# Kernel optimization log

Hardware: AMD Instinct MI355X
Metric: run time of the kernel (lower is better)

## Reference

```python
import jax, jax.numpy as jnp
import numpy as np

N = 100000      # nodes
E_RAND = 1500000
IN_DIM = 128
OUT_DIM = 128
H = 8
D = OUT_DIM // H  # 16 per-head dim
EPS = 1e-5


def _bn(x, gamma, beta):
    # BatchNorm1d, training mode: biased batch statistics over the node dim
    mu = jnp.mean(x, axis=0)
    var = jnp.mean((x - mu) ** 2, axis=0)
    return (x - mu) * jax.lax.rsqrt(var + EPS) * gamma + beta


def setup_inputs() -> dict:
    key = jax.random.key(0)
    ks = jax.random.split(key, 12)
    h = jax.random.normal(ks[0], (N, IN_DIM), dtype=jnp.float32)
    # edge list: random edges + self-loops so every dst has in-degree >= 1
    src_r = jax.random.randint(ks[1], (E_RAND,), 0, N, dtype=jnp.int32)
    dst_r = jax.random.randint(ks[2], (E_RAND,), 0, N, dtype=jnp.int32)
    loops = jnp.arange(N, dtype=jnp.int32)
    src = jnp.concatenate([loops, src_r])
    dst = jnp.concatenate([loops, dst_r])
    s = 1.0 / np.sqrt(IN_DIM)
    Wq = jax.random.normal(ks[3], (IN_DIM, OUT_DIM), dtype=jnp.float32) * s
    Wk = jax.random.normal(ks[4], (IN_DIM, OUT_DIM), dtype=jnp.float32) * s
    Wv = jax.random.normal(ks[5], (IN_DIM, OUT_DIM), dtype=jnp.float32) * s
    Wo = jax.random.normal(ks[6], (OUT_DIM, OUT_DIM), dtype=jnp.float32) * s
    bo = jnp.zeros((OUT_DIM,), dtype=jnp.float32)
    gamma1 = jnp.ones((OUT_DIM,), dtype=jnp.float32)
    beta1 = jnp.zeros((OUT_DIM,), dtype=jnp.float32)
    Wf1 = jax.random.normal(ks[7], (OUT_DIM, 2 * OUT_DIM), dtype=jnp.float32) * s
    bf1 = jnp.zeros((2 * OUT_DIM,), dtype=jnp.float32)
    Wf2 = jax.random.normal(ks[8], (2 * OUT_DIM, OUT_DIM), dtype=jnp.float32) * (1.0 / np.sqrt(2 * OUT_DIM))
    bf2 = jnp.zeros((OUT_DIM,), dtype=jnp.float32)
    gamma2 = jnp.ones((OUT_DIM,), dtype=jnp.float32)
    beta2 = jnp.zeros((OUT_DIM,), dtype=jnp.float32)
    return {"h": h, "Wq": Wq, "Wk": Wk, "Wv": Wv, "Wo": Wo, "bo": bo,
            "gamma1": gamma1, "beta1": beta1, "Wf1": Wf1, "bf1": bf1,
            "Wf2": Wf2, "bf2": bf2, "gamma2": gamma2, "beta2": beta2,
            "src": src, "dst": dst}


def reference(h, Wq, Wk, Wv, Wo, bo, gamma1, beta1, Wf1, bf1, Wf2, bf2,
              gamma2, beta2, src, dst):
    n = h.shape[0]
    Q = (h @ Wq).reshape(n, H, D)
    K = (h @ Wk).reshape(n, H, D)
    V = (h @ Wv).reshape(n, H, D)
    # per-edge score: (K[src] * Q[dst]).sum(-1), scaled exp with clamp
    score = jnp.sum(K[src] * Q[dst], axis=-1) / np.sqrt(D)   # [E, H]
    score = jnp.exp(jnp.clip(score, -5.0, 5.0))
    # weighted aggregation to dst nodes
    wV = jax.ops.segment_sum(V[src] * score[:, :, None], dst, num_segments=n)  # [N,H,D]
    z = jax.ops.segment_sum(score, dst, num_segments=n)                         # [N,H]
    attn = (wV / z[:, :, None]).reshape(n, OUT_DIM)
    # output projection + residual + batchnorm
    x = h + (attn @ Wo + bo)
    x = _bn(x, gamma1, beta1)
    # FFN + residual + batchnorm
    y = jax.nn.relu(x @ Wf1 + bf1) @ Wf2 + bf2
    x = _bn(x + y, gamma2, beta2)
    return x
```

## Files before the change

### kernel.cpp

```cpp
#include <hip/hip_runtime.h>

#define EPS 1e-5f
#define VSCALE 20.0f

typedef __attribute__((ext_vector_type(8))) short sh8;
typedef __attribute__((ext_vector_type(4))) float f4;
typedef __attribute__((ext_vector_type(2))) _Float16 h2f;

static __device__ __forceinline__ unsigned short f2b(float f) {
    union { float f; unsigned u; } v; v.f = f;
    unsigned r = v.u + 0x7FFF + ((v.u >> 16) & 1);
    return (unsigned short)(r >> 16);
}
static __device__ __forceinline__ float b2f(unsigned short b) {
    union { unsigned u; float f; } v; v.u = ((unsigned)b) << 16; return v.f;
}
static __device__ __forceinline__ unsigned pk2(float a, float b) {
    return (unsigned)f2b(a) | ((unsigned)f2b(b) << 16);
}
static __device__ __forceinline__ h2f u2h(unsigned u) {
    union { unsigned u; h2f h; } c; c.u = u; return c.h;
}
static __device__ __forceinline__ unsigned pkh2(float a, float b) {
    union { h2f h; unsigned u; } c;
    c.h.x = (_Float16)a; c.h.y = (_Float16)b;
    return c.u;
}
static __device__ __forceinline__ float dot2h(h2f a, h2f b, float c) {
#if __has_builtin(__builtin_amdgcn_fdot2)
    return __builtin_amdgcn_fdot2(a, b, c, false);
#else
    return (float)a.x * (float)b.x + (float)a.y * (float)b.y + c;
#endif
}
#if __has_builtin(__builtin_amdgcn_cvt_f32_ubyte0)
#define UB0(x) __builtin_amdgcn_cvt_f32_ubyte0(x)
#define UB1(x) __builtin_amdgcn_cvt_f32_ubyte1(x)
#define UB2(x) __builtin_amdgcn_cvt_f32_ubyte2(x)
#define UB3(x) __builtin_amdgcn_cvt_f32_ubyte3(x)
#else
#define UB0(x) ((float)((x) & 0xffu))
#define UB1(x) ((float)(((x) >> 8) & 0xffu))
#define UB2(x) ((float)(((x) >> 16) & 0xffu))
#define UB3(x) ((float)((x) >> 24))
#endif

static __device__ __forceinline__ void barrier_raw() {
    __builtin_amdgcn_sched_barrier(0);
    asm volatile("s_waitcnt lgkmcnt(0)" ::: "memory");
    __builtin_amdgcn_s_barrier();
    __builtin_amdgcn_sched_barrier(0);
}

__global__ __launch_bounds__(256) void prep_all_k(
    const float* __restrict__ Wq, const float* __restrict__ Wk,
    const float* __restrict__ Wv, const float* __restrict__ Wo,
    const float* __restrict__ Wf1, const float* __restrict__ Wf2,
    unsigned short* __restrict__ Wt)
{
    int i = blockIdx.x * 256 + threadIdx.x;
    if (i < 65536) {
        int s = i >> 14;
        const float* W = (s == 0) ? Wq : (s == 1) ? Wk : (s == 2) ? Wv : Wo;
        int l = i & 16383, k = l >> 7, n = l & 127;
        Wt[(i & ~16383) + n * 128 + k] = f2b(W[l]);
    } else if (i < 98304) {
        int l = i - 65536, k = l >> 8, n = l & 255;
        Wt[65536 + n * 128 + k] = f2b(Wf1[l]);
    } else {
        int l = i - 98304, k = l >> 7, n = l & 127;
        Wt[98304 + n * 256 + k] = f2b(Wf2[l]);
    }
}

__global__ __launch_bounds__(512, 4) void qkv3_k(
    const float* __restrict__ h, const unsigned short* __restrict__ Wt,
    _Float16* __restrict__ Qh, unsigned char* __restrict__ KV,
    int M, int tiles)
{
    constexpr int KD = 128, PER = 2;
    __shared__ __align__(16) unsigned short As[2][64 * KD];
    const int tid = threadIdx.x;
    const int wave = tid >> 6, lane = tid & 63;
    const int q = lane >> 4, lm = lane & 15;
    const int wr = wave >> 2, wc = wave & 3;
    const int wv = blockIdx.y;
    const unsigned short* Wblk = Wt + (size_t)wv * 16384;

    float4 rAf[PER][2];
    {
        const int rowT = blockIdx.x * 64;
#pragma unroll
        for (int i = 0; i < PER; ++i) {
            int g = tid + i * 512;
            int row = g >> 4, ch = g & 15;
            int grow = rowT + row; if (grow >= M) grow = M - 1;
            const float* p = &h[(size_t)grow * 128 + ch * 8];
            rAf[i][0] = *(const float4*)p;
            rAf[i][1] = *(const float4*)(p + 4);
        }
    }

    sh8 wfr[2][4];
#pragma unroll
    for (int ni = 0; ni < 2; ++ni)
#pragma unroll
        for (int kc = 0; kc < 4; ++kc)
            wfr[ni][kc] = *(const sh8*)&Wblk[(size_t)(wc * 32 + ni * 16 + lm) * KD
                                             + (kc * 4 + q) * 8];

    int cur = 0;
    for (int t = blockIdx.x; t < tiles; t += gridDim.x) {
        const int rowT = t * 64;
        barrier_raw();
        unsigned short* Asc = As[cur];
#pragma unroll
        for (int i = 0; i < PER; ++i) {
            int g = tid + i * 512;
            int row = g >> 4, ch = g & 15;
            uint4 v;
            v.x = pk2(rAf[i][0].x, rAf[i][0].y);
            v.y = pk2(rAf[i][0].z, rAf[i][0].w);
            v.z = pk2(rAf[i][1].x, rAf[i][1].y);
            v.w = pk2(rAf[i][1].z, rAf[i][1].w);
            *(uint4*)&Asc[row * KD + ((ch ^ (row & 7)) * 8)] = v;
        }
        const int tn = t + (int)gridDim.x;
        if (tn < tiles) {
            const int rowTn = tn * 64;
#pragma unroll
            for (int i = 0; i < PER; ++i) {
                int g = tid + i * 512;
                int row = g >> 4, ch = g & 15;
                int grow = rowTn + row; if (grow >= M) grow = M - 1;
                const float* p = &h[(size_t)grow * 128 + ch * 8];
                rAf[i][0] = *(const float4*)p;
                rAf[i][1] = *(const float4*)(p + 4);
            }
        }
        barrier_raw();

        f4 acc[2][2];
#pragma unroll
        for (int mi = 0; mi < 2; ++mi)
#pragma unroll
            for (int ni = 0; ni < 2; ++ni) {
                f4 z = {0.f, 0.f, 0.f, 0.f};
                acc[mi][ni] = z;
            }
#pragma unroll
        for (int kc = 0; kc < 4; ++kc) {
            sh8 af[2];
#pragma unroll
            for (int mi = 0; mi < 2; ++mi) {
                const int row = wr * 32 + mi * 16 + lm;
                af[mi] = *(const sh8*)&Asc[row * KD + (((kc * 4 + q) ^ (row & 7)) * 8)];
            }
#pragma unroll
            for (int mi = 0; mi < 2; ++mi)
#pragma unroll
                for (int ni = 0; ni < 2; ++ni)
                    acc[mi][ni] = __builtin_amdgcn_mfma_f32_16x16x32_bf16(
                        wfr[ni][kc], af[mi], acc[mi][ni], 0, 0, 0);
        }

#pragma unroll
        for (int mi = 0; mi < 2; ++mi) {
            const int row = rowT + wr * 32 + mi * 16 + lm;
            if (row >= M) continue;
#pragma unroll
            for (int ni = 0; ni < 2; ++ni) {
                const int col0 = wc * 32 + ni * 16 + q * 4;
                const f4 a = acc[mi][ni];
                if (wv == 0) {
                    uint2 o;
                    o.x = pkh2(a[0], a[1]);
                    o.y = pkh2(a[2], a[3]);
                    *(uint2*)&Qh[(size_t)row * 128 + col0] = o;
                } else if (wv == 1) {
                    uint2 o;
                    o.x = pkh2(a[0], a[1]);
                    o.y = pkh2(a[2], a[3]);
                    *(uint2*)(KV + (size_t)row * 384 + col0 * 2) = o;
                } else {
                    unsigned ob = 0;
#pragma unroll
                    for (int r = 0; r < 4; ++r) {
                        float tt = rintf(a[r] * VSCALE);
                        tt = fminf(fmaxf(tt, -127.f), 127.f);
                        ob |= ((unsigned)(unsigned char)(int)(tt + 128.f)) << (r * 8);
                    }
                    *(unsigned*)(KV + (size_t)row * 384 + 256 + col0) = ob;
                }
            }
        }
        cur ^= 1;
    }
}

template<int KD, int RES, int STATS, int RELU>
__global__ __launch_bounds__(512, 4) void gemm3_k(
    const unsigned short* __restrict__ A, const unsigned short* __restrict__ Wt,
    const float* __restrict__ bias, const void* __restrict__ resid,
    unsigned short* __restrict__ C, int M, int ldc, int tiles,
    const float* __restrict__ aff1, float* __restrict__ ostats)
{
    constexpr int CPR = KD / 8;
    constexpr int NWC = (KD == 128) ? 4 : 8;
    constexpr int NI  = (KD == 128) ? 2 : 1;
    constexpr int TM  = (KD == 128) ? 64 : 32;
    constexpr int PER = TM * CPR / 512;
    constexpr int KC  = KD / 32;
    __shared__ __align__(16) unsigned short As[2][TM * KD];
    __shared__ float sacc[256];
    const int tid = threadIdx.x;
    const int wave = tid >> 6, lane = tid & 63;
    const int q = lane >> 4, lm = lane & 15;
    const int wr = wave / NWC, wc = wave % NWC;
    const int colBase = blockIdx.y * 128;
    const unsigned short* Wblk = Wt + (size_t)colBase * KD;

    uint4 rA[PER];
    {
        const int rowT = blockIdx.x * TM;
#pragma unroll
        for (int i = 0; i < PER; ++i) {
            int g = tid + i * 512;
            int row = g / CPR, ch = g % CPR;
            int grow = rowT + row; if (grow >= M) grow = M - 1;
            rA[i] = *(const uint4*)&A[(size_t)grow * KD + ch * 8];
        }
    }

    sh8 wfr[NI][KC];
#pragma unroll
    for (int ni = 0; ni < NI; ++ni)
#pragma unroll
        for (int kc = 0; kc < KC; ++kc)
            wfr[ni][kc] = *(const sh8*)&Wblk[(size_t)(wc * (16 * NI) + ni * 16 + lm) * KD
                                             + (kc * 4 + q) * 8];
    if (STATS && tid < 256) sacc[tid] = 0.f;

    float4 bv4[NI], rsc4[NI], rsh4[NI];
#pragma unroll
    for (int ni = 0; ni < NI; ++ni) {
        const int col0 = colBase + wc * (16 * NI) + ni * 16 + q * 4;
        bv4[ni] = *(const float4*)&bias[col0];
        if (RES == 3) {
            rsc4[ni] = *(const float4*)&aff1[col0];
            rsh4[ni] = *(const float4*)&aff1[128 + col0];
        } else {
            rsc4[ni] = make_float4(0.f, 0.f, 0.f, 0.f);
            rsh4[ni] = make_float4(0.f, 0.f, 0.f, 0.f);
        }
    }
    f4 st_s[NI], st_ss[NI];
#pragma unroll
    for (int ni = 0; ni < NI; ++ni) {
        f4 z = {0.f, 0.f, 0.f, 0.f};
        st_s[ni] = z; st_ss[ni] = z;
    }

    int cur = 0;
    for (int t = blockIdx.x; t < tiles; t += gridDim.x) {
        const int rowT = t * TM;
        barrier_raw();
        unsigned short* Asc = As[cur];
#pragma unroll
        for (int i = 0; i < PER; ++i) {
            int g = tid + i * 512;
            int row = g / CPR, ch = g % CPR;
            *(uint4*)&Asc[row * KD + ((ch ^ (row & 7)) * 8)] = rA[i];
        }
        const int tn = t + (int)gridDim.x;
        if (tn < tiles) {
            const int rowTn = tn * TM;
#pragma unroll
            for (int i = 0; i < PER; ++i) {
                int g = tid + i * 512;
                int row = g / CPR, ch = g % CPR;
                int grow = rowTn + row; if (grow >= M) grow = M - 1;
                rA[i] = *(const uint4*)&A[(size_t)grow * KD + ch * 8];
            }
        }
        barrier_raw();

        f4 acc[2][NI];
#pragma unroll
        for (int mi = 0; mi < 2; ++mi)
#pragma unroll
            for (int ni = 0; ni < NI; ++ni) {
                f4 z = {0.f, 0.f, 0.f, 0.f};
                acc[mi][ni] = z;
            }
#pragma unroll
        for (int kc = 0; kc < KC; ++kc) {
            sh8 af[2];
#pragma unroll
            for (int mi = 0; mi < 2; ++mi) {
                const int row = wr * 32 + mi * 16 + lm;
                af[mi] = *(const sh8*)&Asc[row * KD + (((kc * 4 + q) ^ (row & 7)) * 8)];
            }
#pragma unroll
            for (int mi = 0; mi < 2; ++mi)
#pragma unroll
                for (int ni = 0; ni < NI; ++ni)
                    acc[mi][ni] = __builtin_amdgcn_mfma_f32_16x16x32_bf16(
                        wfr[ni][kc], af[mi], acc[mi][ni], 0, 0, 0);
        }

#pragma unroll
        for (int mi = 0; mi < 2; ++mi) {
            const int row = rowT + wr * 32 + mi * 16 + lm;
            if (row >= M) continue;
#pragma unroll
            for (int ni = 0; ni < NI; ++ni) {
                const int col0 = colBase + wc * (16 * NI) + ni * 16 + q * 4;
                const size_t rb = (size_t)row * ldc + col0;
                const f4 a = acc[mi][ni];
                float v0 = a[0] + bv4[ni].x, v1 = a[1] + bv4[ni].y;
                float v2 = a[2] + bv4[ni].z, v3 = a[3] + bv4[ni].w;
                if (RES == 1) {
                    const float4 rv = *(const float4*)&((const float*)resid)[rb];
                    v0 += rv.x; v1 += rv.y; v2 += rv.z; v3 += rv.w;
                }
                if (RES == 3) {
                    const uint2 rv = *(const uint2*)&((const unsigned short*)resid)[rb];
                    v0 += b2f((unsigned short)(rv.x & 0xffff)) * rsc4[ni].x + rsh4[ni].x;
                    v1 += b2f((unsigned short)(rv.x >> 16))    * rsc4[ni].y + rsh4[ni].y;
                    v2 += b2f((unsigned short)(rv.y & 0xffff)) * rsc4[ni].z + rsh4[ni].z;
                    v3 += b2f((unsigned short)(rv.y >> 16))    * rsc4[ni].w + rsh4[ni].w;
                }
                if (RELU) {
                    v0 = fmaxf(v0, 0.f); v1 = fmaxf(v1, 0.f);
                    v2 = fmaxf(v2, 0.f); v3 = fmaxf(v3, 0.f);
                }
                if (STATS) {
                    st_s[ni][0] += v0; st_s[ni][1] += v1;
                    st_s[ni][2] += v2; st_s[ni][3] += v3;
                    st_ss[ni][0] += v0 * v0; st_ss[ni][1] += v1 * v1;
                    st_ss[ni][2] += v2 * v2; st_ss[ni][3] += v3 * v3;
                }
                uint2 o;
                o.x = pk2(v0, v1); o.y = pk2(v2, v3);
                *(uint2*)&C[rb] = o;
            }
        }
        cur ^= 1;
    }

    if (STATS) {
        barrier_raw();
#pragma unroll
        for (int ni = 0; ni < NI; ++ni) {
#pragma unroll
            for (int m = 1; m <= 8; m <<= 1) {
#pragma unroll
                for (int r = 0; r < 4; ++r) {
                    st_s[ni][r]  += __shfl_xor(st_s[ni][r], m);
                    st_ss[ni][r] += __shfl_xor(st_ss[ni][r], m);
                }
            }
            if (lm == 0) {
                const int col0 = wc * (16 * NI) + ni * 16 + q * 4;
#pragma unroll
                for (int r = 0; r < 4; ++r) {
                    atomicAdd(&sacc[col0 + r], st_s[ni][r]);
                    atomicAdd(&sacc[128 + col0 + r], st_ss[ni][r]);
                }
            }
        }
        barrier_raw();
        if (tid < 128) {
            atomicAdd(&ostats[tid], sacc[tid]);
            atomicAdd(&ostats[128 + tid], sacc[128 + tid]);
        }
    }
}

__global__ __launch_bounds__(256) void fold_bn1_k(
    const unsigned short* __restrict__ W1t, const float* __restrict__ rstats,
    const float* __restrict__ g1, const float* __restrict__ b1,
    const float* __restrict__ bf1, float invN,
    unsigned short* __restrict__ W1f, float* __restrict__ b1f,
    float* __restrict__ aff1)
{
    __shared__ float sc[128], sh[128];
    const int t = threadIdx.x;
    if (t < 128) {
        const float mu = rstats[t] * invN;
        const float var = rstats[128 + t] * invN - mu * mu;
        const float isg = rsqrtf(var + EPS) * g1[t];
        const float shf = b1[t] - mu * isg;
        sc[t] = isg; sh[t] = shf;
        aff1[t] = isg; aff1[128 + t] = shf;
    }
    __syncthreads();
    float acc = bf1[t];
#pragma unroll
    for (int c = 0; c < 128; c += 8) {
        const uint4 v = *(const uint4*)&W1t[t * 128 + c];
        const float w0 = b2f((unsigned short)(v.x & 0xffff));
        const float w1 = b2f((unsigned short)(v.x >> 16));
        const float w2 = b2f((unsigned short)(v.y & 0xffff));
        const float w3 = b2f((unsigned short)(v.y >> 16));
        const float w4 = b2f((unsigned short)(v.z & 0xffff));
        const float w5 = b2f((unsigned short)(v.z >> 16));
        const float w6 = b2f((unsigned short)(v.w & 0xffff));
        const float w7 = b2f((unsigned short)(v.w >> 16));
        acc += sh[c] * w0 + sh[c + 1] * w1 + sh[c + 2] * w2 + sh[c + 3] * w3
             + sh[c + 4] * w4 + sh[c + 5] * w5 + sh[c + 6] * w6 + sh[c + 7] * w7;
        uint4 o;
        o.x = pk2(w0 * sc[c],     w1 * sc[c + 1]);
        o.y = pk2(w2 * sc[c + 2], w3 * sc[c + 3]);
        o.z = pk2(w4 * sc[c + 4], w5 * sc[c + 5]);
        o.w = pk2(w6 * sc[c + 6], w7 * sc[c + 7]);
        *(uint4*)&W1f[t * 128 + c] = o;
    }
    b1f[t] = acc;
}

__global__ __launch_bounds__(256) void bucket_cnt_k(const int* __restrict__ dst,
                                                    int E, int* __restrict__ bCnt)
{
    __shared__ int c[512];
    const int t = threadIdx.x;
    c[t] = 0; c[t + 256] = 0;
    __syncthreads();
    for (int i = blockIdx.x * 256 + t; i < E; i += gridDim.x * 256)
        atomicAdd(&c[dst[i] >> 8], 1);
    __syncthreads();
    if (c[t]) atomicAdd(&bCnt[t], c[t]);
    if (c[t + 256]) atomicAdd(&bCnt[t + 256], c[t + 256]);
}

__global__ __launch_bounds__(512) void bucket_scan_k(const int* __restrict__ bCnt,
                                                     int B, int* __restrict__ bOff,
                                                     int* __restrict__ bCur)
{
    __shared__ int ts[512];
    const int t = threadIdx.x;
    const int v = (t < B) ? bCnt[t] : 0;
    ts[t] = v;
    __syncthreads();
    for (int o = 1; o < 512; o <<= 1) {
        int u = (t >= o) ? ts[t - o] : 0;
        __syncthreads();
        ts[t] += u;
        __syncthreads();
    }
    const int ex = ts[t] - v;
    if (t < B) { bOff[t] = ex; bCur[t] = ex; }
    if (t == B - 1) bOff[B] = ex + v;
}

#define CCH 8192
__global__ __launch_bounds__(512) void coarse_k(const int* __restrict__ src,
                                                const int* __restrict__ dst, int E,
                                                int* __restrict__ bCur,
                                                unsigned* __restrict__ coarse)
{
    __shared__ int cnt[512], off[512], gbase[512], rc[512];
    __shared__ unsigned pk[CCH];
    __shared__ int ga[CCH];
    const int t = threadIdx.x;
    const int e0 = blockIdx.x * CCH;
    const int n = min(CCH, E - e0);
    cnt[t] = 0;
    __syncthreads();
    for (int i = t; i < n; i += 512) atomicAdd(&cnt[dst[e0 + i] >> 8], 1);
    __syncthreads();
    const int v = cnt[t];
    off[t] = v;
    __syncthreads();
    for (int o = 1; o < 512; o <<= 1) {
        int u = (t >= o) ? off[t - o] : 0;
        __syncthreads();
        off[t] += u;
        __syncthreads();
    }
    const int ex = off[t] - v;
    off[t] = ex;
    if (v > 0) gbase[t] = atomicAdd(&bCur[t], v);
    rc[t] = 0;
    __syncthreads();
    for (int i = t; i < n; i += 512) {
        const int d = dst[e0 + i], s = src[e0 + i];
        const int b = d >> 8;
        const int j = atomicAdd(&rc[b], 1);
        const int slot = off[b] + j;
        pk[slot] = ((unsigned)(d & 255) << 17) | (unsigned)s;
        ga[slot] = gbase[b] + j;
    }
    __syncthreads();
    for (int i = t; i < n; i += 512) coarse[ga[i]] = pk[i];
}

__global__ __launch_bounds__(256) void fine_k(const unsigned* __restrict__ coarse,
                                              const int* __restrict__ bOff, int B,
                                              int Nn, int* __restrict__ row_ptr,
                                              int* __restrict__ esrc)
{
    __shared__ int cnt[256], off[256], rc[256];
    const int t = threadIdx.x;
    const int b = blockIdx.x;
    const int base = b << 8;
    const int e0 = bOff[b], e1 = bOff[b + 1];
    cnt[t] = 0;
    __syncthreads();
    for (int i = e0 + t; i < e1; i += 256)
        atomicAdd(&cnt[(coarse[i] >> 17) & 255], 1);
    __syncthreads();
    const int v = cnt[t];
    off[t] = v;
    __syncthreads();
    for (int o = 1; o < 256; o <<= 1) {
        int u = (t >= o) ? off[t - o] : 0;
        __syncthreads();
        off[t] += u;
        __syncthreads();
    }
    const int ex = off[t] - v;
    off[t] = ex;
    rc[t] = 0;
    if (base + t < Nn) row_ptr[base + t] = e0 + ex;
    if (b == B - 1 && t == 0) row_ptr[Nn] = e1;
    __syncthreads();
    for (int i = e0 + t; i < e1; i += 256) {
        const unsigned p = coarse[i];
        const int l = (p >> 17) & 255;
        const int j = atomicAdd(&rc[l], 1);
        esrc[e0 + off[l] + j] = (int)(p & 0x1FFFFu);
    }
}

#define EA_ACC(kc, vc, EI) do {                                              \
    float sp = dot2h(u2h((kc).w), q3, dot2h(u2h((kc).z), q2,                 \
               dot2h(u2h((kc).y), q1, dot2h(u2h((kc).x), q0, 0.f))));        \
    sp += __shfl_xor(sp, 1);                                                 \
    float sc = __expf(fminf(fmaxf(sp * 0.25f, -5.f), 5.f));                  \
    sc = ((EI) < nb) ? sc : 0.f;                                             \
    a0 += sc * UB0((vc).x);                                                  \
    a1 += sc * UB1((vc).x);                                                  \
    a2 += sc * UB2((vc).x);                                                  \
    a3 += sc * UB3((vc).x);                                                  \
    a4 += sc * UB0((vc).y);                                                  \
    a5 += sc * UB1((vc).y);                                                  \
    a6 += sc * UB2((vc).y);                                                  \
    a7 += sc * UB3((vc).y);                                                  \
    z += sc;                                                                 \
} while (0)

__global__ __launch_bounds__(256) void edge_attn_k(
    const _Float16* __restrict__ Qh, const unsigned char* __restrict__ KV,
    const int* __restrict__ row_ptr, const int* __restrict__ esrc,
    unsigned short* __restrict__ attnb, int nodeOff, int nodeEnd)
{
    const int wave = threadIdx.x >> 6, lane = threadIdx.x & 63;
    const int node = nodeOff + blockIdx.x * 4 + wave;
    if (node >= nodeEnd) return;
    const int g = lane & 15, p = lane >> 4;
    const uint4 qv = *(const uint4*)&Qh[(size_t)node * 128 + g * 8];
    const h2f q0 = u2h(qv.x), q1 = u2h(qv.y), q2 = u2h(qv.z), q3 = u2h(qv.w);
    const int e0 = row_ptr[node], e1 = row_ptr[node + 1];
    const int cnt = e1 - e0;
    const int e1m1 = e1 - 1;
    float a0 = 0.f, a1 = 0.f, a2 = 0.f, a3 = 0.f;
    float a4 = 0.f, a5 = 0.f, a6 = 0.f, a7 = 0.f, z = 0.f;
    for (int base = 0; base < cnt; base += 64) {
        const int nb = min(cnt - base, 64);
        const int eb = e0 + base + p;
        {
            const int s0 = esrc[min(eb, e1m1)];
            const unsigned char* r = KV + (size_t)((unsigned)s0 * 384u);
            const int s1 = esrc[min(eb + 4, e1m1)];
            const unsigned char* rB = KV + (size_t)((unsigned)s1 * 384u);
            uint4 kvA = *(const uint4*)(r + g * 16);
            uint2 vvA = *(const uint2*)(r + 256 + g * 8);
            uint4 kvB = *(const uint4*)(rB + g * 16);
            uint2 vvB = *(const uint2*)(rB + 256 + g * 8);
            for (int j = 0; j < nb; j += 8) {
                {
                    const uint4 kc = kvA; const uint2 vc = vvA;
                    if (j + 8 < nb) {
                        const int sn = esrc[min(eb + j + 8, e1m1)];
                        const unsigned char* rn = KV + (size_t)((unsigned)sn * 384u);
                        kvA = *(const uint4*)(rn + g * 16);
                        vvA = *(const uint2*)(rn + 256 + g * 8);
                    }
                    EA_ACC(kc, vc, j + p);
                }
                {
                    const uint4 kc = kvB; const uint2 vc = vvB;
                    if (j + 12 < nb) {
                        const int sn = esrc[min(eb + j + 12, e1m1)];
                        const unsigned char* rn = KV + (size_t)((unsigned)sn * 384u);
                        kvB = *(const uint4*)(rn + g * 16);
                        vvB = *(const uint2*)(rn + 256 + g * 8);
                    }
                    EA_ACC(kc, vc, j + 4 + p);
                }
            }
        }
    }
    a0 += __shfl_xor(a0, 16); a0 += __shfl_xor(a0, 32);
    a1 += __shfl_xor(a1, 16); a1 += __shfl_xor(a1, 32);
    a2 += __shfl_xor(a2, 16); a2 += __shfl_xor(a2, 32);
    a3 += __shfl_xor(a3, 16); a3 += __shfl_xor(a3, 32);
    a4 += __shfl_xor(a4, 16); a4 += __shfl_xor(a4, 32);
    a5 += __shfl_xor(a5, 16); a5 += __shfl_xor(a5, 32);
    a6 += __shfl_xor(a6, 16); a6 += __shfl_xor(a6, 32);
    a7 += __shfl_xor(a7, 16); a7 += __shfl_xor(a7, 32);
    z  += __shfl_xor(z, 16);  z  += __shfl_xor(z, 32);
    const float inv = 1.f / (z * VSCALE);
    const float c = 128.f * z;
    if (p == 0) {
        uint4 o;
        o.x = pk2((a0 - c) * inv, (a1 - c) * inv);
        o.y = pk2((a2 - c) * inv, (a3 - c) * inv);
        o.z = pk2((a4 - c) * inv, (a5 - c) * inv);
        o.w = pk2((a6 - c) * inv, (a7 - c) * inv);
        *(uint4*)&attnb[(size_t)node * 128 + g * 8] = o;
    }
}

__global__ __launch_bounds__(256) void bn_apply_b_k(const unsigned short* __restrict__ X,
                                                    const float* __restrict__ rstats,
                                                    const float* __restrict__ gma,
                                                    const float* __restrict__ bta,
                                                    float invN, int total8,
                                                    float* __restrict__ out)
{
    __shared__ float aff[256];
    if (threadIdx.x < 128) {
        const int c = threadIdx.x;
        const float mu = rstats[c] * invN;
        const float var = rstats[128 + c] * invN - mu * mu;
        const float isg = rsqrtf(var + EPS) * gma[c];
        aff[c] = isg;
        aff[128 + c] = bta[c] - mu * isg;
    }
    __syncthreads();
    for (int i = blockIdx.x * blockDim.x + threadIdx.x; i < total8;
         i += gridDim.x * blockDim.x) {
        const int c8 = (i & 15) * 8;
        const float4 sc0 = *(const float4*)&aff[c8];
        const float4 sc1 = *(const float4*)&aff[c8 + 4];
        const float4 sh0 = *(const float4*)&aff[128 + c8];
        const float4 sh1 = *(const float4*)&aff[128 + c8 + 4];
        const uint4 v = ((const uint4*)X)[i];
        float4 o0, o1;
        o0.x = b2f((unsigned short)(v.x & 0xffff)) * sc0.x + sh0.x;
        o0.y = b2f((unsigned short)(v.x >> 16))    * sc0.y + sh0.y;
        o0.z = b2f((unsigned short)(v.y & 0xffff)) * sc0.z + sh0.z;
        o0.w = b2f((unsigned short)(v.y >> 16))    * sc0.w + sh0.w;
        o1.x = b2f((unsigned short)(v.z & 0xffff)) * sc1.x + sh1.x;
        o1.y = b2f((unsigned short)(v.z >> 16))    * sc1.y + sh1.y;
        o1.z = b2f((unsigned short)(v.w & 0xffff)) * sc1.z + sh1.z;
        o1.w = b2f((unsigned short)(v.w >> 16))    * sc1.w + sh1.w;
        ((float4*)out)[i * 2]     = o0;
        ((float4*)out)[i * 2 + 1] = o1;
    }
}

extern "C" void kernel_launch(void* const* d_in, const int* in_sizes, int n_in,
                              void* d_out, int out_size, void* d_ws, size_t ws_size,
                              hipStream_t stream)
{
    const float* h   = (const float*)d_in[0];
    const float* Wq  = (const float*)d_in[1];
    const float* Wk  = (const float*)d_in[2];
    const float* Wv  = (const float*)d_in[3];
    const float* Wo  = (const float*)d_in[4];
    const float* bo  = (const float*)d_in[5];
    const float* g1  = (const float*)d_in[6];
    const float* b1  = (const float*)d_in[7];
    const float* Wf1 = (const float*)d_in[8];
    const float* bf1 = (const float*)d_in[9];
    const float* Wf2 = (const float*)d_in[10];
    const float* bf2 = (const float*)d_in[11];
    const float* g2  = (const float*)d_in[12];
    const float* b2  = (const float*)d_in[13];
    const int*   src = (const int*)d_in[14];
    const int*   dstv= (const int*)d_in[15];
    const int N = in_sizes[0] / 128;
    const int E = in_sizes[14];
    const int B = (N + 255) >> 8;
    const float invN = 1.f / (float)N;

    unsigned short* Wt = (unsigned short*)d_ws;
    float* stats1 = (float*)((char*)d_ws + 262144);
    float* stats2 = stats1 + 256;
    int* bCnt = (int*)(stats2 + 256);
    int* bOff = bCnt + 512;
    int* bCur = bOff + 513;
    uintptr_t big = ((uintptr_t)(bCur + 512) + 255) & ~(uintptr_t)255;
    _Float16* Qh = (_Float16*)big;
    unsigned char* KV = (unsigned char*)(Qh + (size_t)N * 128);
    uintptr_t a2 = ((uintptr_t)(KV + (size_t)N * 384) + 255) & ~(uintptr_t)255;
    unsigned short* attnb = (unsigned short*)a2;
    unsigned short* xb = attnb + (size_t)N * 128;
    int* row_ptr = (int*)(xb + (size_t)N * 128);
    unsigned* coarse = (unsigned*)attnb;
    int* esrc = (int*)xb;
    unsigned short* hidden = (unsigned short*)Qh;
    unsigned short* yb = attnb;
    uintptr_t fb = (big + (size_t)N * 512 + 255) & ~(uintptr_t)255;
    float* aff1 = (float*)fb;
    float* b1f  = aff1 + 256;
    unsigned short* W1f = (unsigned short*)(b1f + 256);

    unsigned short* Wf1T = Wt + 65536;
    unsigned short* Wf2T = Wt + 98304;

    float* out = (float*)d_out;
    const dim3 b256(256);
    const dim3 b512(512);
    const int tiles64 = (N + 63) / 64;
    const int tiles32 = (N + 31) / 32;

    hipMemsetAsync(stats1, 0, 4096, stream);

    prep_all_k<<<dim3(512), b256, 0, stream>>>(Wq, Wk, Wv, Wo, Wf1, Wf2, Wt);

    bucket_cnt_k<<<dim3(256), b256, 0, stream>>>(dstv, E, bCnt);
    bucket_scan_k<<<dim3(1), dim3(512), 0, stream>>>(bCnt, B, bOff, bCur);
    coarse_k<<<dim3((E + CCH - 1) / CCH), dim3(512), 0, stream>>>(src, dstv, E, bCur, coarse);
    fine_k<<<dim3(B), b256, 0, stream>>>(coarse, bOff, B, N, row_ptr, esrc);

    qkv3_k<<<dim3(341, 3), b512, 0, stream>>>(h, Wt, Qh, KV, N, tiles64);

    edge_attn_k<<<dim3((N + 3) / 4), b256, 0, stream>>>(
        Qh, KV, row_ptr, esrc, attnb, 0, N);

    gemm3_k<128, 1, 1, 0><<<dim3(512, 1), b512, 0, stream>>>(
        attnb, Wt + 49152, bo, h, xb, N, 128, tiles64, nullptr, stats1);

    fold_bn1_k<<<dim3(1), b256, 0, stream>>>(Wf1T, stats1, g1, b1, bf1, invN,
                                             W1f, b1f, aff1);

    gemm3_k<128, 0, 0, 1><<<dim3(512, 2), b512, 0, stream>>>(
        xb, W1f, b1f, nullptr, hidden, N, 256, tiles64, nullptr, nullptr);

    gemm3_k<256, 3, 1, 0><<<dim3(512, 1), b512, 0, stream>>>(
        hidden, Wf2T, bf2, xb, yb, N, 128, tiles32, aff1, stats2);

    bn_apply_b_k<<<dim3(1024), b256, 0, stream>>>(yb, stats2, g2, b2, invN, N * 16, out);
}
```

Before: 439.4 us.

## Compute all QKV columns per block and widen FFN1 tiles to full N

The QKV projection now has each block compute all 384 output columns (Q, K, V) for a 32-row tile, each wave holding 48 columns of weights. Before, a 3-wide grid re-read and re-converted the same fp32 h tile once per projection. The FFN1 GEMM is likewise templated to cover all 256 output columns per block with 32-row tiles, so the A tile is loaded once instead of twice. The trade is more registers per wave for the larger weight fragment and accumulator sets, plus smaller row tiles and more loop iterations.

```diff
diff --git a/kernel.cpp b/kernel.cpp
--- a/kernel.cpp
+++ b/kernel.cpp
@@ -78,73 +78,61 @@
     _Float16* __restrict__ Qh, unsigned char* __restrict__ KV,
     int M, int tiles)
 {
-    constexpr int KD = 128, PER = 2;
-    __shared__ __align__(16) unsigned short As[2][64 * KD];
+    constexpr int KD = 128;
+    __shared__ __align__(16) unsigned short As[2][32 * KD];
     const int tid = threadIdx.x;
     const int wave = tid >> 6, lane = tid & 63;
     const int q = lane >> 4, lm = lane & 15;
-    const int wr = wave >> 2, wc = wave & 3;
-    const int wv = blockIdx.y;
-    const unsigned short* Wblk = Wt + (size_t)wv * 16384;
-
-    float4 rAf[PER][2];
+    const int wc = wave;
+
+    float4 rAf[2];
     {
-        const int rowT = blockIdx.x * 64;
-#pragma unroll
-        for (int i = 0; i < PER; ++i) {
-            int g = tid + i * 512;
-            int row = g >> 4, ch = g & 15;
-            int grow = rowT + row; if (grow >= M) grow = M - 1;
-            const float* p = &h[(size_t)grow * 128 + ch * 8];
-            rAf[i][0] = *(const float4*)p;
-            rAf[i][1] = *(const float4*)(p + 4);
-        }
-    }
-
-    sh8 wfr[2][4];
-#pragma unroll
-    for (int ni = 0; ni < 2; ++ni)
+        const int rowT = blockIdx.x * 32;
+        int row = tid >> 4, ch = tid & 15;
+        int grow = rowT + row; if (grow >= M) grow = M - 1;
+        const float* p = &h[(size_t)grow * 128 + ch * 8];
+        rAf[0] = *(const float4*)p;
+        rAf[1] = *(const float4*)(p + 4);
+    }
+
+    sh8 wfr[3][4];
+#pragma unroll
+    for (int ni = 0; ni < 3; ++ni)
 #pragma unroll
         for (int kc = 0; kc < 4; ++kc)
-            wfr[ni][kc] = *(const sh8*)&Wblk[(size_t)(wc * 32 + ni * 16 + lm) * KD
-                                             + (kc * 4 + q) * 8];
+            wfr[ni][kc] = *(const sh8*)&Wt[(size_t)(wc * 48 + ni * 16 + lm) * KD
+                                           + (kc * 4 + q) * 8];
 
     int cur = 0;
     for (int t = blockIdx.x; t < tiles; t += gridDim.x) {
-        const int rowT = t * 64;
+        const int rowT = t * 32;
         barrier_raw();
         unsigned short* Asc = As[cur];
-#pragma unroll
-        for (int i = 0; i < PER; ++i) {
-            int g = tid + i * 512;
-            int row = g >> 4, ch = g & 15;
+        {
+            int row = tid >> 4, ch = tid & 15;
             uint4 v;
-            v.x = pk2(rAf[i][0].x, rAf[i][0].y);
-            v.y = pk2(rAf[i][0].z, rAf[i][0].w);
-            v.z = pk2(rAf[i][1].x, rAf[i][1].y);
-            v.w = pk2(rAf[i][1].z, rAf[i][1].w);
+            v.x = pk2(rAf[0].x, rAf[0].y);
+            v.y = pk2(rAf[0].z, rAf[0].w);
+            v.z = pk2(rAf[1].x, rAf[1].y);
+            v.w = pk2(rAf[1].z, rAf[1].w);
             *(uint4*)&Asc[row * KD + ((ch ^ (row & 7)) * 8)] = v;
         }
         const int tn = t + (int)gridDim.x;
         if (tn < tiles) {
-            const int rowTn = tn * 64;
-#pragma unroll
-            for (int i = 0; i < PER; ++i) {
-                int g = tid + i * 512;
-                int row = g >> 4, ch = g & 15;
-                int grow = rowTn + row; if (grow >= M) grow = M - 1;
-                const float* p = &h[(size_t)grow * 128 + ch * 8];
-                rAf[i][0] = *(const float4*)p;
-                rAf[i][1] = *(const float4*)(p + 4);
-            }
+            const int rowTn = tn * 32;
+            int row = tid >> 4, ch = tid & 15;
+            int grow = rowTn + row; if (grow >= M) grow = M - 1;
+            const float* p = &h[(size_t)grow * 128 + ch * 8];
+            rAf[0] = *(const float4*)p;
+            rAf[1] = *(const float4*)(p + 4);
         }
         barrier_raw();
 
-        f4 acc[2][2];
+        f4 acc[2][3];
 #pragma unroll
         for (int mi = 0; mi < 2; ++mi)
 #pragma unroll
-            for (int ni = 0; ni < 2; ++ni) {
+            for (int ni = 0; ni < 3; ++ni) {
                 f4 z = {0.f, 0.f, 0.f, 0.f};
                 acc[mi][ni] = z;
             }
@@ -153,35 +141,37 @@
             sh8 af[2];
 #pragma unroll
             for (int mi = 0; mi < 2; ++mi) {
-                const int row = wr * 32 + mi * 16 + lm;
+                const int row = mi * 16 + lm;
                 af[mi] = *(const sh8*)&Asc[row * KD + (((kc * 4 + q) ^ (row & 7)) * 8)];
             }
 #pragma unroll
             for (int mi = 0; mi < 2; ++mi)
 #pragma unroll
-                for (int ni = 0; ni < 2; ++ni)
+                for (int ni = 0; ni < 3; ++ni)
                     acc[mi][ni] = __builtin_amdgcn_mfma_f32_16x16x32_bf16(
                         wfr[ni][kc], af[mi], acc[mi][ni], 0, 0, 0);
         }
 
 #pragma unroll
         for (int mi = 0; mi < 2; ++mi) {
-            const int row = rowT + wr * 32 + mi * 16 + lm;
+            const int row = rowT + mi * 16 + lm;
             if (row >= M) continue;
 #pragma unroll
-            for (int ni = 0; ni < 2; ++ni) {
-                const int col0 = wc * 32 + ni * 16 + q * 4;
+            for (int ni = 0; ni < 3; ++ni) {
+                const int colg = wc * 48 + ni * 16 + q * 4;
+                const int prod = colg >> 7;
+                const int lc = colg & 127;
                 const f4 a = acc[mi][ni];
-                if (wv == 0) {
+                if (prod == 0) {
                     uint2 o;
                     o.x = pkh2(a[0], a[1]);
                     o.y = pkh2(a[2], a[3]);
-                    *(uint2*)&Qh[(size_t)row * 128 + col0] = o;
-                } else if (wv == 1) {
+                    *(uint2*)&Qh[(size_t)row * 128 + lc] = o;
+                } else if (prod == 1) {
                     uint2 o;
                     o.x = pkh2(a[0], a[1]);
                     o.y = pkh2(a[2], a[3]);
-                    *(uint2*)(KV + (size_t)row * 384 + col0 * 2) = o;
+                    *(uint2*)(KV + (size_t)row * 384 + lc * 2) = o;
                 } else {
                     unsigned ob = 0;
 #pragma unroll
@@ -190,7 +180,7 @@
                         tt = fminf(fmaxf(tt, -127.f), 127.f);
                         ob |= ((unsigned)(unsigned char)(int)(tt + 128.f)) << (r * 8);
                     }
-                    *(unsigned*)(KV + (size_t)row * 384 + 256 + col0) = ob;
+                    *(unsigned*)(KV + (size_t)row * 384 + 256 + lc) = ob;
                 }
             }
         }
@@ -198,7 +188,7 @@
     }
 }
 
-template<int KD, int RES, int STATS, int RELU>
+template<int KD, int NCOL, int RES, int STATS, int RELU>
 __global__ __launch_bounds__(512, 4) void gemm3_k(
     const unsigned short* __restrict__ A, const unsigned short* __restrict__ Wt,
     const float* __restrict__ bias, const void* __restrict__ resid,
@@ -206,9 +196,9 @@
     const float* __restrict__ aff1, float* __restrict__ ostats)
 {
     constexpr int CPR = KD / 8;
-    constexpr int NWC = (KD == 128) ? 4 : 8;
     constexpr int NI  = (KD == 128) ? 2 : 1;
-    constexpr int TM  = (KD == 128) ? 64 : 32;
+    constexpr int NWC = NCOL / (16 * NI);
+    constexpr int TM  = 256 / NWC;
     constexpr int PER = TM * CPR / 512;
     constexpr int KC  = KD / 32;
     __shared__ __align__(16) unsigned short As[2][TM * KD];
@@ -217,7 +207,7 @@
     const int wave = tid >> 6, lane = tid & 63;
     const int q = lane >> 4, lm = lane & 15;
     const int wr = wave / NWC, wc = wave % NWC;
-    const int colBase = blockIdx.y * 128;
+    const int colBase = blockIdx.y * NCOL;
     const unsigned short* Wblk = Wt + (size_t)colBase * KD;
 
     uint4 rA[PER];
@@ -728,21 +718,21 @@
     coarse_k<<<dim3((E + CCH - 1) / CCH), dim3(512), 0, stream>>>(src, dstv, E, bCur, coarse);
     fine_k<<<dim3(B), b256, 0, stream>>>(coarse, bOff, B, N, row_ptr, esrc);
 
-    qkv3_k<<<dim3(341, 3), b512, 0, stream>>>(h, Wt, Qh, KV, N, tiles64);
+    qkv3_k<<<dim3(1024), b512, 0, stream>>>(h, Wt, Qh, KV, N, tiles32);
 
     edge_attn_k<<<dim3((N + 3) / 4), b256, 0, stream>>>(
         Qh, KV, row_ptr, esrc, attnb, 0, N);
 
-    gemm3_k<128, 1, 1, 0><<<dim3(512, 1), b512, 0, stream>>>(
+    gemm3_k<128, 128, 1, 1, 0><<<dim3(512, 1), b512, 0, stream>>>(
         attnb, Wt + 49152, bo, h, xb, N, 128, tiles64, nullptr, stats1);
 
     fold_bn1_k<<<dim3(1), b256, 0, stream>>>(Wf1T, stats1, g1, b1, bf1, invN,
                                              W1f, b1f, aff1);
 
-    gemm3_k<128, 0, 0, 1><<<dim3(512, 2), b512, 0, stream>>>(
-        xb, W1f, b1f, nullptr, hidden, N, 256, tiles64, nullptr, nullptr);
-
-    gemm3_k<256, 3, 1, 0><<<dim3(512, 1), b512, 0, stream>>>(
+    gemm3_k<128, 256, 0, 0, 1><<<dim3(512, 1), b512, 0, stream>>>(
+        xb, W1f, b1f, nullptr, hidden, N, 256, tiles32, nullptr, nullptr);
+
+    gemm3_k<256, 128, 3, 1, 0><<<dim3(512, 1), b512, 0, stream>>>(
         hidden, Wf2T, bf2, xb, yb, N, 128, tiles32, aff1, stats2);
 
     bn_apply_b_k<<<dim3(1024), b256, 0, stream>>>(yb, stats2, g2, b2, invN, N * 16, out);
```

Result: faster. 419.1 us (-4.6%).
